# Kernel optimization log

Measured on AMD Instinct MI355X. Metric: run time of the kernel, lower is better.

Reference implementation:

```python
import jax, jax.numpy as jnp
import numpy as np

B, L, E, H = 4, 512, 2048, 32
S = E // H  # head_size = 64
EXTRA_MAA, EXTRA_DECAY = 32, 64
EPS = 1e-5


def setup_inputs() -> dict:
    key = jax.random.key(0)
    ks = jax.random.split(key, 24)
    rn = lambda k, shp, s=1.0: jax.random.normal(k, shp, dtype=jnp.float32) * s
    return dict(
        x=rn(ks[0], (B, L, E)),
        state=rn(ks[1], (B, 2 + S, E), 0.1),
        ln1_w=jnp.ones((E,), jnp.float32), ln1_b=jnp.zeros((E,), jnp.float32),
        ln2_w=jnp.ones((E,), jnp.float32), ln2_b=jnp.zeros((E,), jnp.float32),
        maa_x=rn(ks[2], (E,), 0.02),
        maa_w1=rn(ks[3], (E, 5 * EXTRA_MAA), 0.02),
        maa_w2=rn(ks[4], (5, EXTRA_MAA, E), 0.02),
        maa_stack=rn(ks[5], (5, E), 0.02),          # [k,w,v,r,g] time_maa vectors
        time_decay=rn(ks[6], (E,), 0.5),
        decay_w1=rn(ks[7], (E, EXTRA_DECAY), 0.02),
        decay_w2=rn(ks[8], (EXTRA_DECAY, E), 0.02),
        faaaa=rn(ks[9], (H, S), 0.1),
        Wr=rn(ks[10], (E, E), 0.02), Wk=rn(ks[11], (E, E), 0.02),
        Wv=rn(ks[12], (E, E), 0.02), Wg=rn(ks[13], (E, E), 0.02),
        Wo=rn(ks[14], (E, E), 0.02),
        gn_w=jnp.ones((E,), jnp.float32), gn_b=jnp.zeros((E,), jnp.float32),
        ffn_maa_k=rn(ks[15], (E,), 0.02), ffn_maa_r=rn(ks[16], (E,), 0.02),
        ffn_Wk=rn(ks[17], (E, E), 0.02), ffn_Wr=rn(ks[18], (E, E), 0.02),
        ffn_Wv=rn(ks[19], (E, E), 0.02),
        i=0,
    )


def _ln(x, w, b):
    m = jnp.mean(x, axis=-1, keepdims=True)
    v = jnp.mean((x - m) ** 2, axis=-1, keepdims=True)
    return (x - m) * jax.lax.rsqrt(v + EPS) * w + b


def _token_shift(xn, prev_row):
    # sx_lerp[t] = x[t-1] - x[t], with state row as x[-1]
    first = (prev_row - xn[:, 0])[:, None]
    rest = xn[:, :-1] - xn[:, 1:]
    return jnp.concatenate([first, rest], axis=1)


def reference(x, state, ln1_w, ln1_b, ln2_w, ln2_b, maa_x, maa_w1, maa_w2,
              maa_stack, time_decay, decay_w1, decay_w2, faaaa,
              Wr, Wk, Wv, Wg, Wo, gn_w, gn_b,
              ffn_maa_k, ffn_maa_r, ffn_Wk, ffn_Wr, ffn_Wv, i):
    b, l = x.shape[0], x.shape[1]
    i0 = (2 + S) * i + 0
    i1 = (2 + S) * i + 1

    # ---- time mixing (parallel) ----
    xn = _ln(x, ln1_w, ln1_b)
    sx = _token_shift(xn, state[:, i1])
    xxx = jnp.tanh((xn + sx * maa_x) @ maa_w1).reshape(b, l, 5, 1, EXTRA_MAA)
    xxx = jnp.matmul(xxx, maa_w2).reshape(b, l, 5, E)   # [B,L,5,E]
    x5 = xn[:, :, None] + sx[:, :, None] * (maa_stack + xxx)

    w = jnp.exp(-jnp.exp(time_decay + jnp.tanh(x5[:, :, 1] @ decay_w1) @ decay_w2))
    w = w.reshape(b, l, H, S)
    r = (x5[:, :, 3] @ Wr.T).reshape(b, l, H, S)
    k = (x5[:, :, 0] @ Wk.T).reshape(b, l, H, S)
    v = (x5[:, :, 2] @ Wv.T).reshape(b, l, H, S)
    g = jax.nn.silu(x5[:, :, 4] @ Wg.T)                 # [B,L,E]

    s0 = state[:, (2 + S) * i + 2:(2 + S) * (i + 1)].reshape(b, H, S, S)
    u = faaaa[None, :, :, None]                         # [1,H,S,1]

    def step(s, rkvw):
        r_t, k_t, v_t, w_t = rkvw                      # each [B,H,S]
        a = k_t[:, :, :, None] * v_t[:, :, None, :]    # [B,H,S,S] outer product
        out = jnp.einsum('bhk,bhkd->bhd', r_t, u * a + s)
        return a + w_t[:, :, :, None] * s, out

    xs = tuple(jnp.moveaxis(t, 1, 0) for t in (r, k, v, w))
    _, outs = jax.lax.scan(step, s0, xs)               # outs [L,B,H,S]
    att = jnp.moveaxis(outs, 0, 1).reshape(b, l, E)

    # group norm over each head's channels
    a4 = att.reshape(b, l, H, S)
    m = jnp.mean(a4, axis=-1, keepdims=True)
    var = jnp.mean((a4 - m) ** 2, axis=-1, keepdims=True)
    att = ((a4 - m) * jax.lax.rsqrt(var + EPS)).reshape(b, l, E) * gn_w + gn_b
    x = x + (att * g) @ Wo.T

    # ---- channel mixing (parallel) ----
    xn2 = _ln(x, ln2_w, ln2_b)
    sx2 = _token_shift(xn2, state[:, i0])
    xk = xn2 + sx2 * ffn_maa_k
    xr = xn2 + sx2 * ffn_maa_r
    rr = jax.nn.sigmoid(xr @ ffn_Wr.T)
    kk = jnp.square(jax.nn.relu(xk @ ffn_Wk.T))
    x = x + rr * (kk @ ffn_Wv.T)
    return x
```

## Files before the change

kernel.cpp:

```cpp
#include <hip/hip_runtime.h>

#define EE 2048
#define LL 512
#define BBATCH 4
#define HH 32
#define SS 64
#define EPSF 1e-5f
static constexpr size_t NEL = (size_t)BBATCH * LL * EE;

typedef __attribute__((ext_vector_type(8))) short short8;
typedef __attribute__((ext_vector_type(4))) float f32x4;

__device__ __forceinline__ unsigned short f2bf(float f) {
  union { float f; unsigned u; } x; x.f = f;
  return (unsigned short)((x.u + 0x7fffu + ((x.u >> 16) & 1u)) >> 16);
}

__device__ __forceinline__ void gload_lds16(const unsigned short* g, unsigned short* l) {
  __builtin_amdgcn_global_load_lds((const __attribute__((address_space(1))) void*)g,
                                   (__attribute__((address_space(3))) void*)l, 16, 0, 0);
}

template <int N>
__device__ __forceinline__ void wait_vmcnt_n() {
  if constexpr (N == 4) asm volatile("s_waitcnt vmcnt(4)" ::: "memory");
  else if constexpr (N == 6) asm volatile("s_waitcnt vmcnt(6)" ::: "memory");
  else if constexpr (N == 8) asm volatile("s_waitcnt vmcnt(8)" ::: "memory");
  else asm volatile("s_waitcnt vmcnt(0)" ::: "memory");
}

struct CvArgs {
  const float* s[4];
  unsigned short* d[4];
};
__global__ void __launch_bounds__(256) f2bf_batch(CvArgs a, int n4) {
  int z = blockIdx.y;
  int idx = blockIdx.x * 256 + threadIdx.x;
  if (idx >= n4) return;
  float4 v = ((const float4*)a.s[z])[idx];
  ushort4 o;
  o.x = f2bf(v.x); o.y = f2bf(v.y); o.z = f2bf(v.z); o.w = f2bf(v.w);
  ((ushort4*)a.d[z])[idx] = o;
}

__global__ void __launch_bounds__(256) wprep_kernel(const float* __restrict__ w1,
                                                    const float* __restrict__ w2,
                                                    const float* __restrict__ d1,
                                                    const float* __restrict__ d2,
                                                    unsigned short* __restrict__ w1T,
                                                    unsigned short* __restrict__ w2cat,
                                                    unsigned short* __restrict__ dw1T,
                                                    unsigned short* __restrict__ dw2T) {
  const int N0 = 256 * 2048;
  const int N1 = 10240 * 160;
  const int N2 = 128 * 2048;
  const int N3 = 2048 * 128;
  int id = blockIdx.x * 256 + threadIdx.x;
  if (id < N0) {
    int n = id >> 11, k = id & 2047;
    float v = (n < 160) ? w1[(size_t)k * 160 + n] : 0.f;
    w1T[id] = f2bf(v);
    return;
  }
  id -= N0;
  if (id < N1) {
    int n = id / 160, kq = id - n * 160;
    int j = n >> 11, e = n & 2047;
    float v = ((kq >> 5) == j) ? w2[(size_t)kq * 2048 + e] : 0.f;
    w2cat[id] = f2bf(v);
    return;
  }
  id -= N1;
  if (id < N2) {
    int n = id >> 11, k = id & 2047;
    float v = (n < 64) ? d1[(size_t)k * 64 + n] : 0.f;
    dw1T[id] = f2bf(v);
    return;
  }
  id -= N2;
  if (id < N3) {
    int n = id >> 7, k = id & 127;
    float v = (k < 64) ? d2[(size_t)k * 2048 + n] : 0.f;
    dw2T[id] = f2bf(v);
  }
}

template <int SIDE>
__global__ void __launch_bounds__(256) ln_shift_kernel(
    const float* __restrict__ x, const float* __restrict__ state, const int* __restrict__ ip,
    const float* __restrict__ lnw, const float* __restrict__ lnb,
    const float* __restrict__ mA, const float* __restrict__ mB,
    float* __restrict__ xn_out, unsigned short* __restrict__ o1,
    float* __restrict__ sx_out, unsigned short* __restrict__ o2) {
  __shared__ float red[8];
  int tok = blockIdx.x;
  int b = tok >> 9, t = tok & 511;
  int tid = threadIdx.x;
  int e = tid * 8;
  size_t base = (size_t)tok * EE;
  float c[8], p[8];
  *(float4*)&c[0] = *(const float4*)&x[base + e];
  *(float4*)&c[4] = *(const float4*)&x[base + e + 4];
  bool hasp = (t != 0);
  if (hasp) {
    *(float4*)&p[0] = *(const float4*)&x[base - EE + e];
    *(float4*)&p[4] = *(const float4*)&x[base - EE + e + 4];
  } else {
    const float* srow = state + ((size_t)b * (2 + SS) + (size_t)(2 + SS) * (*ip) +
                                 (SIDE == 0 ? 1 : 0)) * EE;
    *(float4*)&p[0] = *(const float4*)&srow[e];
    *(float4*)&p[4] = *(const float4*)&srow[e + 4];
  }
  float sc = 0.f, sp = 0.f;
#pragma unroll
  for (int j = 0; j < 8; ++j) { sc += c[j]; sp += p[j]; }
#pragma unroll
  for (int off = 32; off >= 1; off >>= 1) {
    sc += __shfl_xor(sc, off);
    sp += __shfl_xor(sp, off);
  }
  if ((tid & 63) == 0) { red[tid >> 6] = sc; red[4 + (tid >> 6)] = sp; }
  __syncthreads();
  float mc = (red[0] + red[1] + red[2] + red[3]) * (1.f / EE);
  float mp = (red[4] + red[5] + red[6] + red[7]) * (1.f / EE);
  __syncthreads();
  float qc = 0.f, qp = 0.f;
#pragma unroll
  for (int j = 0; j < 8; ++j) {
    float dc = c[j] - mc, dp = p[j] - mp;
    qc += dc * dc; qp += dp * dp;
  }
#pragma unroll
  for (int off = 32; off >= 1; off >>= 1) {
    qc += __shfl_xor(qc, off);
    qp += __shfl_xor(qp, off);
  }
  if ((tid & 63) == 0) { red[tid >> 6] = qc; red[4 + (tid >> 6)] = qp; }
  __syncthreads();
  float rc = rsqrtf((red[0] + red[1] + red[2] + red[3]) * (1.f / EE) + EPSF);
  float rp = rsqrtf((red[4] + red[5] + red[6] + red[7]) * (1.f / EE) + EPSF);
  float wv[8], bv[8], av[8], bv2[8];
  *(float4*)&wv[0] = *(const float4*)&lnw[e];
  *(float4*)&wv[4] = *(const float4*)&lnw[e + 4];
  *(float4*)&bv[0] = *(const float4*)&lnb[e];
  *(float4*)&bv[4] = *(const float4*)&lnb[e + 4];
  *(float4*)&av[0] = *(const float4*)&mA[e];
  *(float4*)&av[4] = *(const float4*)&mA[e + 4];
  if (SIDE == 1) {
    *(float4*)&bv2[0] = *(const float4*)&mB[e];
    *(float4*)&bv2[4] = *(const float4*)&mB[e + 4];
  }
  float cn[8], sxv[8];
#pragma unroll
  for (int j = 0; j < 8; ++j) {
    float cnj = (c[j] - mc) * rc * wv[j] + bv[j];
    float pnj = hasp ? ((p[j] - mp) * rp * wv[j] + bv[j]) : p[j];
    cn[j] = cnj;
    sxv[j] = pnj - cnj;
  }
  if constexpr (SIDE == 0) {
    *(float4*)&xn_out[base + e] = *(float4*)&cn[0];
    *(float4*)&xn_out[base + e + 4] = *(float4*)&cn[4];
    *(float4*)&sx_out[base + e] = *(float4*)&sxv[0];
    *(float4*)&sx_out[base + e + 4] = *(float4*)&sxv[4];
    ushort4 xo0, xo1;
    xo0.x = f2bf(cn[0] + sxv[0] * av[0]); xo0.y = f2bf(cn[1] + sxv[1] * av[1]);
    xo0.z = f2bf(cn[2] + sxv[2] * av[2]); xo0.w = f2bf(cn[3] + sxv[3] * av[3]);
    xo1.x = f2bf(cn[4] + sxv[4] * av[4]); xo1.y = f2bf(cn[5] + sxv[5] * av[5]);
    xo1.z = f2bf(cn[6] + sxv[6] * av[6]); xo1.w = f2bf(cn[7] + sxv[7] * av[7]);
    *(ushort4*)&o1[base + e] = xo0;
    *(ushort4*)&o1[base + e + 4] = xo1;
  } else {
    ushort4 k0, k1, r0, r1;
    k0.x = f2bf(cn[0] + sxv[0] * av[0]); k0.y = f2bf(cn[1] + sxv[1] * av[1]);
    k0.z = f2bf(cn[2] + sxv[2] * av[2]); k0.w = f2bf(cn[3] + sxv[3] * av[3]);
    k1.x = f2bf(cn[4] + sxv[4] * av[4]); k1.y = f2bf(cn[5] + sxv[5] * av[5]);
    k1.z = f2bf(cn[6] + sxv[6] * av[6]); k1.w = f2bf(cn[7] + sxv[7] * av[7]);
    r0.x = f2bf(cn[0] + sxv[0] * bv2[0]); r0.y = f2bf(cn[1] + sxv[1] * bv2[1]);
    r0.z = f2bf(cn[2] + sxv[2] * bv2[2]); r0.w = f2bf(cn[3] + sxv[3] * bv2[3]);
    r1.x = f2bf(cn[4] + sxv[4] * bv2[4]); r1.y = f2bf(cn[5] + sxv[5] * bv2[5]);
    r1.z = f2bf(cn[6] + sxv[6] * bv2[6]); r1.w = f2bf(cn[7] + sxv[7] * bv2[7]);
    *(ushort4*)&o1[base + e] = k0;
    *(ushort4*)&o1[base + e + 4] = k1;
    *(ushort4*)&o2[base + e] = r0;
    *(ushort4*)&o2[base + e + 4] = r1;
  }
}

template <int ROWS, int BK, int NT>
__device__ __forceinline__ void stage_mat(const unsigned short* __restrict__ base, int ld,
                                          int k0, unsigned short* dst) {
  constexpr int GPR = BK / 8;
  constexpr int L = ROWS * GPR / NT;
  int tid = threadIdx.x;
#pragma unroll
  for (int r = 0; r < L; ++r) {
    int g = r * NT + tid;
    int row = g / GPR, p = g & (GPR - 1);
    int lg = p ^ (row & (GPR - 1));
    gload_lds16(base + (size_t)row * ld + k0 + lg * 8, &dst[g * 8]);
  }
}

template <int BM, int BN, int BK, int NT, int WM, int WN>
__device__ __forceinline__ void gemm_core(const unsigned short* __restrict__ A, int lda,
                                          const unsigned short* __restrict__ W, int ldw,
                                          int K, int bm, int bn, unsigned short* AsAll,
                                          unsigned short* BsAll,
                                          f32x4 (&acc)[BM / WM / 16][BN / WN / 16],
                                          int& m0o, int& n0o) {
  constexpr int FM = BM / WM / 16, FN = BN / WN / 16, KS = BK / 32;
  constexpr int GPR = BK / 8;
  constexpr int NLD = (BM + BN) * GPR / NT;
  int tid = threadIdx.x;
  int wave = tid >> 6, lane = tid & 63;
  int wm = wave / WN, wn = wave % WN;
  const unsigned short* Abase = A + (size_t)bm * BM * lda;
  const unsigned short* Bbase = W + (size_t)bn * BN * ldw;
  const int T = K / BK;
  stage_mat<BM, BK, NT>(Abase, lda, 0, AsAll);
  stage_mat<BN, BK, NT>(Bbase, ldw, 0, BsAll);
  {
    int k1 = (T > 1) ? BK : 0;
    stage_mat<BM, BK, NT>(Abase, lda, k1, AsAll + BM * BK);
    stage_mat<BN, BK, NT>(Bbase, ldw, k1, BsAll + BN * BK);
  }
  int q = lane >> 4;
  int rA = wm * (BM / WM) + (lane & 15);
  int rB = wn * (BN / WN) + (lane & 15);
  int xrA = rA & (GPR - 1), xrB = rB & (GPR - 1);
  for (int t = 0; t < T; ++t) {
    unsigned short* As = AsAll + (t & 1) * (BM * BK);
    unsigned short* Bs = BsAll + (t & 1) * (BN * BK);
    wait_vmcnt_n<NLD>();
    __builtin_amdgcn_s_barrier();
    __builtin_amdgcn_sched_barrier(0);
    short8 av[KS][FM], bv[KS][FN];
#pragma unroll
    for (int ks = 0; ks < KS; ++ks) {
#pragma unroll
      for (int f = 0; f < FM; f++) {
        int p = (ks * 4 + q) ^ xrA;
        av[ks][f] = *(const short8*)&As[(rA + f * 16) * BK + p * 8];
      }
#pragma unroll
      for (int f = 0; f < FN; f++) {
        int p = (ks * 4 + q) ^ xrB;
        bv[ks][f] = *(const short8*)&Bs[(rB + f * 16) * BK + p * 8];
      }
    }
    asm volatile("s_waitcnt lgkmcnt(0)" ::: "memory");
    __builtin_amdgcn_sched_barrier(0);
    __builtin_amdgcn_s_barrier();
    int tn = t + 2;
    if (tn >= T) tn -= T;
    stage_mat<BM, BK, NT>(Abase, lda, tn * BK, As);
    stage_mat<BN, BK, NT>(Bbase, ldw, tn * BK, Bs);
    __builtin_amdgcn_s_setprio(1);
#pragma unroll
    for (int ks = 0; ks < KS; ++ks)
#pragma unroll
      for (int fm = 0; fm < FM; fm++)
#pragma unroll
        for (int fn = 0; fn < FN; fn++)
          acc[fm][fn] = __builtin_amdgcn_mfma_f32_16x16x32_bf16(av[ks][fm], bv[ks][fn],
                                                                acc[fm][fn], 0, 0, 0);
    __builtin_amdgcn_s_setprio(0);
  }
  m0o = bm * BM + wm * (BM / WM);
  n0o = bn * BN + wn * (BN / WN);
}

template <int FM, int FN, typename F>
__device__ __forceinline__ void epi_loop(f32x4 (&acc)[FM][FN], int m0, int n0, F f) {
  int lane = threadIdx.x & 63;
  int rl = (lane >> 4) * 4, cl = lane & 15;
#pragma unroll
  for (int fm = 0; fm < FM; fm++)
#pragma unroll
    for (int fn = 0; fn < FN; fn++)
#pragma unroll
      for (int q = 0; q < 4; q++)
        f(m0 + fm * 16 + rl + q, n0 + fn * 16 + cl, acc[fm][fn][q]);
}

template <int MODE, int BM, int BN, int BK>
__global__ void __launch_bounds__(256) gemm_bt(const unsigned short* __restrict__ A, int lda,
                                               const unsigned short* __restrict__ W, int ldw,
                                               int K, int NB, void* __restrict__ Cout, int ldc,
                                               const float* __restrict__ p1,
                                               const float* __restrict__ p2,
                                               const float* __restrict__ p3) {
  __shared__ __align__(16) unsigned short As[2 * BM * BK];
  __shared__ __align__(16) unsigned short Bs[2 * BN * BK];
  int nwg = gridDim.x, bid = blockIdx.x;
  int qd = nwg >> 3;
  int wg = (bid & 7) * qd + (bid >> 3);
  int bm = wg / NB, bn = wg - bm * NB;
  f32x4 acc[BM / 32][BN / 32] = {};
  int m0, n0;
  gemm_core<BM, BN, BK, 256, 2, 2>(A, lda, W, ldw, K, bm, bn, As, Bs, acc, m0, n0);
  epi_loop(acc, m0, n0, [&](int m, int n, float val) {
    size_t o = (size_t)m * ldc + n;
    if constexpr (MODE == 2) {
      ((float*)Cout)[o] = p1[o] + val;
    } else if constexpr (MODE == 3) {
      ((float*)Cout)[o] = p1[o] + val * (1.f / (1.f + expf(-p2[o])));
    } else if constexpr (MODE == 5) {
      ((unsigned short*)Cout)[o] = f2bf(tanhf(val));
    } else if constexpr (MODE == 6) {
      ((float*)Cout)[o] = expf(-expf(p1[n] + val));
    } else {
      int j = n >> 11, e = n & 2047;
      size_t oe = (size_t)m * EE + e;
      float xv = p1[oe];
      float sv = p2[oe];
      float st = p3[(size_t)j * EE + e];
      ((unsigned short*)Cout)[(size_t)j * NEL + oe] = f2bf(xv + sv * (st + val));
    }
  });
}

struct Proj4Args {
  const unsigned short* A[4];
  const unsigned short* W[4];
  float* C[4];
};
__global__ void __launch_bounds__(512, 1) gemm_proj4(Proj4Args args) {
  __shared__ __align__(16) unsigned short As[2 * 256 * 64];
  __shared__ __align__(16) unsigned short Bs[2 * 256 * 64];
  int bid = blockIdx.x;
  int xcd = bid & 7;
  int z = xcd >> 1;
  int tile = ((xcd & 1) << 5) + (bid >> 3);
  int bm = tile >> 3, bn = tile & 7;
  f32x4 acc[8][4] = {};
  int m0, n0;
  gemm_core<256, 256, 64, 512, 2, 4>(args.A[z], EE, args.W[z], EE, EE, bm, bn, As, Bs, acc,
                                     m0, n0);
  float* C = args.C[z];
  bool silu = (z == 3);
  epi_loop(acc, m0, n0, [&](int m, int n, float val) {
    size_t o = (size_t)m * EE + n;
    C[o] = silu ? (val / (1.f + expf(-val))) : val;
  });
}

__global__ void __launch_bounds__(256) gemm_ffn2(const unsigned short* A0,
                                                 const unsigned short* A1,
                                                 const unsigned short* W0,
                                                 const unsigned short* W1, float* C0,
                                                 unsigned short* C1) {
  __shared__ __align__(16) unsigned short As[2 * 128 * 64];
  __shared__ __align__(16) unsigned short Bs[2 * 128 * 64];
  int bid = blockIdx.x;
  int xcd = bid & 7;
  int z = xcd >> 2;
  int tile = ((xcd & 3) << 6) + (bid >> 3);
  int bm = tile >> 4, bn = tile & 15;
  f32x4 acc[4][4] = {};
  int m0, n0;
  gemm_core<128, 128, 64, 256, 2, 2>(z ? A1 : A0, EE, z ? W1 : W0, EE, EE, bm, bn, As, Bs,
                                     acc, m0, n0);
  epi_loop(acc, m0, n0, [&](int m, int n, float val) {
    size_t o = (size_t)m * EE + n;
    if (z == 0) {
      C0[o] = val;
    } else {
      float rv = fmaxf(val, 0.f);
      C1[o] = f2bf(rv * rv);
    }
  });
}

__global__ void __launch_bounds__(512) scan_kernel(const float* __restrict__ r,
                                                   const float* __restrict__ k,
                                                   const float* __restrict__ v,
                                                   const float* __restrict__ w,
                                                   const float* __restrict__ state,
                                                   const float* __restrict__ faaaa,
                                                   const int* __restrict__ ip,
                                                   float* __restrict__ att) {
  __shared__ float bR[2][8][32], bK[2][8][32], bW[2][8][32];
  __shared__ float bV[2][8][64];
  __shared__ float part[8][8][64];
  int blk = blockIdx.x;
  int bh = blk >> 1, kh = blk & 1;
  int b = bh >> 5, h = bh & 31;
  int tid = threadIdx.x, wv = tid >> 6, lane = tid & 63;
  int klocal = wv * 4;
  int k0w = kh * 32 + klocal;
  int ii = *ip;
  const float* sb = state + ((size_t)b * (2 + SS) + (size_t)(2 + SS) * ii + 2) * EE;
  float s_[4], u_[4];
#pragma unroll
  for (int q = 0; q < 4; ++q) {
    int kk_ = k0w + q;
    s_[q] = sb[(size_t)(2 * h + (kk_ >> 5)) * EE + (kk_ & 31) * 64 + lane];
    u_[q] = faaaa[h * 64 + kk_];
  }
  size_t base = (size_t)b * LL * EE + (size_t)h * 64;
  int c = tid;
  bool ld = c < 320;
  int lt = c / 40, r40 = c - lt * 40;
  int la = (r40 < 24) ? (r40 >> 3) : 3;
  int lcG = (r40 < 24) ? (kh * 32 + (r40 & 7) * 4) : ((r40 - 24) * 4);
  int lcL = (r40 < 24) ? ((r40 & 7) * 4) : ((r40 - 24) * 4);
  const float* lsrc = nullptr;
  if (ld) {
    const float* arr = (la == 0) ? r : (la == 1) ? k : (la == 2) ? w : v;
    lsrc = arr + base + (size_t)lt * EE + lcG;
    float4 v0 = *(const float4*)lsrc;
    if (la == 0) *(float4*)&bR[0][lt][lcL] = v0;
    else if (la == 1) *(float4*)&bK[0][lt][lcL] = v0;
    else if (la == 2) *(float4*)&bW[0][lt][lcL] = v0;
    else *(float4*)&bV[0][lt][lcL] = v0;
  }
  __syncthreads();
  for (int g = 0; g < 64; ++g) {
    int cb = g & 1;
    float4 nv;
    if (ld && g < 63) nv = *(const float4*)(lsrc + (size_t)(g + 1) * 8 * EE);
#pragma unroll
    for (int t = 0; t < 8; ++t) {
      float vv = bV[cb][t][lane];
      float acc = 0.f;
#pragma unroll
      for (int q = 0; q < 4; ++q) {
        float rk = bR[cb][t][klocal + q];
        float kk2 = bK[cb][t][klocal + q];
        float wk = bW[cb][t][klocal + q];
        float a = kk2 * vv;
        acc = fmaf(rk, fmaf(u_[q], a, s_[q]), acc);
        s_[q] = fmaf(wk, s_[q], a);
      }
      part[t][wv][lane] = acc;
    }
    if (ld && g < 63) {
      int nb = cb ^ 1;
      if (la == 0) *(float4*)&bR[nb][lt][lcL] = nv;
      else if (la == 1) *(float4*)&bK[nb][lt][lcL] = nv;
      else if (la == 2) *(float4*)&bW[nb][lt][lcL] = nv;
      else *(float4*)&bV[nb][lt][lcL] = nv;
    }
    __syncthreads();
    {
      int t = tid >> 6, d = tid & 63;
      float tot = part[t][0][d] + part[t][1][d] + part[t][2][d] + part[t][3][d] +
                  part[t][4][d] + part[t][5][d] + part[t][6][d] + part[t][7][d];
      atomicAdd(&att[base + (size_t)(g * 8 + t) * EE + d], tot);
    }
    __syncthreads();
  }
}

__global__ void __launch_bounds__(256) gn_gate_kernel(const float* __restrict__ att,
                                                      const float* __restrict__ g,
                                                      const float* __restrict__ gnw,
                                                      const float* __restrict__ gnb,
                                                      unsigned short* __restrict__ attg) {
  int tok = blockIdx.x, tid = threadIdx.x;
  int h = tid >> 3, j = tid & 7;
  size_t base = (size_t)tok * EE + h * 64 + j * 8;
  int e = h * 64 + j * 8;
  float4 a0 = *(const float4*)&att[base];
  float4 a1 = *(const float4*)&att[base + 4];
  float s = a0.x + a0.y + a0.z + a0.w + a1.x + a1.y + a1.z + a1.w;
  s += __shfl_xor(s, 1); s += __shfl_xor(s, 2); s += __shfl_xor(s, 4);
  float mean = s * (1.f / 64.f);
  float d, q = 0.f;
  d = a0.x - mean; q += d * d; d = a0.y - mean; q += d * d;
  d = a0.z - mean; q += d * d; d = a0.w - mean; q += d * d;
  d = a1.x - mean; q += d * d; d = a1.y - mean; q += d * d;
  d = a1.z - mean; q += d * d; d = a1.w - mean; q += d * d;
  q += __shfl_xor(q, 1); q += __shfl_xor(q, 2); q += __shfl_xor(q, 4);
  float rstd = rsqrtf(q * (1.f / 64.f) + EPSF);
  float4 w0 = *(const float4*)&gnw[e], w1 = *(const float4*)&gnw[e + 4];
  float4 b0 = *(const float4*)&gnb[e], b1 = *(const float4*)&gnb[e + 4];
  float4 g0 = *(const float4*)&g[base], g1 = *(const float4*)&g[base + 4];
  ushort4 o0, o1;
  o0.x = f2bf(((a0.x - mean) * rstd * w0.x + b0.x) * g0.x);
  o0.y = f2bf(((a0.y - mean) * rstd * w0.y + b0.y) * g0.y);
  o0.z = f2bf(((a0.z - mean) * rstd * w0.z + b0.z) * g0.z);
  o0.w = f2bf(((a0.w - mean) * rstd * w0.w + b0.w) * g0.w);
  o1.x = f2bf(((a1.x - mean) * rstd * w1.x + b1.x) * g1.x);
  o1.y = f2bf(((a1.y - mean) * rstd * w1.y + b1.y) * g1.y);
  o1.z = f2bf(((a1.z - mean) * rstd * w1.z + b1.z) * g1.z);
  o1.w = f2bf(((a1.w - mean) * rstd * w1.w + b1.w) * g1.w);
  *(ushort4*)&attg[base] = o0;
  *(ushort4*)&attg[base + 4] = o1;
}

extern "C" void kernel_launch(void* const* d_in, const int* in_sizes, int n_in,
                              void* d_out, int out_size, void* d_ws, size_t ws_size,
                              hipStream_t stream) {
  const float* x = (const float*)d_in[0];
  const float* state = (const float*)d_in[1];
  const float* ln1_w = (const float*)d_in[2];
  const float* ln1_b = (const float*)d_in[3];
  const float* ln2_w = (const float*)d_in[4];
  const float* ln2_b = (const float*)d_in[5];
  const float* maa_x = (const float*)d_in[6];
  const float* maa_w1 = (const float*)d_in[7];
  const float* maa_w2 = (const float*)d_in[8];
  const float* maa_stack = (const float*)d_in[9];
  const float* time_decay = (const float*)d_in[10];
  const float* decay_w1 = (const float*)d_in[11];
  const float* decay_w2 = (const float*)d_in[12];
  const float* faaaa = (const float*)d_in[13];
  const float* Wr = (const float*)d_in[14];
  const float* Wk = (const float*)d_in[15];
  const float* Wv = (const float*)d_in[16];
  const float* Wg = (const float*)d_in[17];
  const float* Wo = (const float*)d_in[18];
  const float* gn_w = (const float*)d_in[19];
  const float* gn_b = (const float*)d_in[20];
  const float* ffn_maa_k = (const float*)d_in[21];
  const float* ffn_maa_r = (const float*)d_in[22];
  const float* fWk = (const float*)d_in[23];
  const float* fWr = (const float*)d_in[24];
  const float* fWv = (const float*)d_in[25];
  const int* ip = (const int*)d_in[26];

  char* ws = (char*)d_ws;
  const size_t MB1 = 1024 * 1024;
  unsigned short* WB0 = (unsigned short*)ws;
  unsigned short* WB1 = (unsigned short*)(ws + 8 * MB1);
  float* xn = (float*)(ws + 16 * MB1);
  unsigned short* x5b = (unsigned short*)(ws + 32 * MB1);
  float* wbuf = (float*)(ws + 72 * MB1);
  float* rbuf = (float*)(ws + 88 * MB1);
  float* kbuf = (float*)(ws + 104 * MB1);
  float* vbuf = (float*)(ws + 120 * MB1);
  float* gbuf = (float*)(ws + 136 * MB1);
  char* smalls = ws + 152 * MB1;
  unsigned short* th = (unsigned short*)smalls;
  unsigned short* w1T = (unsigned short*)(smalls + 1 * MB1);
  unsigned short* w2cat = (unsigned short*)(smalls + 2 * MB1);
  unsigned short* dw1T = (unsigned short*)(smalls + 5376 * 1024);
  unsigned short* dw2T = (unsigned short*)(smalls + 5888 * 1024);
  unsigned short* dt = (unsigned short*)(smalls + 6400 * 1024);

  unsigned short* xxm = (unsigned short*)wbuf;
  float* sx = gbuf;
  float* att = xn;
  unsigned short* WB2 = (unsigned short*)xn;
  unsigned short* WB3 = WB2 + NEL;
  unsigned short* attg = x5b;
  unsigned short* xkb = x5b;
  unsigned short* fWvB = x5b + 1 * NEL;
  unsigned short* xrb = x5b + 2 * NEL;
  unsigned short* kkb = x5b + 3 * NEL;
  unsigned short* fWkB = x5b + 4 * NEL;
  float* rrraw = wbuf;

  const int thr = 256;
  const int nconv = (int)(NEL / 4);

  ln_shift_kernel<0><<<BBATCH * LL, thr, 0, stream>>>(x, state, ip, ln1_w, ln1_b, maa_x,
                                                      nullptr, xn, xxm, sx, nullptr);
  wprep_kernel<<<10496, thr, 0, stream>>>(maa_w1, maa_w2, decay_w1, decay_w2, w1T, w2cat,
                                          dw1T, dw2T);
  gemm_bt<5, 64, 64, 64><<<128, thr, 0, stream>>>(xxm, 2048, w1T, 2048, 2048, 4, th, 256,
                                                  nullptr, nullptr, nullptr);
  gemm_bt<7, 128, 128, 32><<<1280, thr, 0, stream>>>(th, 256, w2cat, 160, 160, 80, x5b, 0,
                                                     xn, sx, maa_stack);
  gemm_bt<5, 64, 64, 64><<<64, thr, 0, stream>>>(x5b + 1 * NEL, 2048, dw1T, 2048, 2048, 2,
                                                 dt, 128, nullptr, nullptr, nullptr);
  gemm_bt<6, 128, 128, 64><<<256, thr, 0, stream>>>(dt, 128, dw2T, 128, 128, 16, wbuf, 2048,
                                                    time_decay, nullptr, nullptr);
  {
    CvArgs ca;
    ca.s[0] = Wk; ca.d[0] = WB0;
    ca.s[1] = Wv; ca.d[1] = WB1;
    ca.s[2] = Wr; ca.d[2] = WB2;
    ca.s[3] = Wg; ca.d[3] = WB3;
    f2bf_batch<<<dim3(4096, 4), thr, 0, stream>>>(ca, nconv);
  }
  {
    Proj4Args pa;
    pa.A[0] = x5b + 0 * NEL; pa.W[0] = WB0; pa.C[0] = kbuf;
    pa.A[1] = x5b + 2 * NEL; pa.W[1] = WB1; pa.C[1] = vbuf;
    pa.A[2] = x5b + 3 * NEL; pa.W[2] = WB2; pa.C[2] = rbuf;
    pa.A[3] = x5b + 4 * NEL; pa.W[3] = WB3; pa.C[3] = gbuf;
    gemm_proj4<<<256, 512, 0, stream>>>(pa);
  }
  {
    CvArgs cb;
    cb.s[0] = Wo; cb.d[0] = WB0;
    cb.s[1] = fWr; cb.d[1] = WB1;
    cb.s[2] = fWk; cb.d[2] = fWkB;
    cb.s[3] = fWv; cb.d[3] = fWvB;
    f2bf_batch<<<dim3(4096, 4), thr, 0, stream>>>(cb, nconv);
  }
  (void)hipMemsetAsync(att, 0, NEL * sizeof(float), stream);
  scan_kernel<<<256, 512, 0, stream>>>(rbuf, kbuf, vbuf, wbuf, state, faaaa, ip, att);
  gn_gate_kernel<<<BBATCH * LL, thr, 0, stream>>>(att, gbuf, gn_w, gn_b, attg);
  gemm_bt<2, 128, 64, 64><<<512, thr, 0, stream>>>(attg, 2048, WB0, 2048, 2048, 32,
                                                   (float*)d_out, 2048, x, nullptr, nullptr);
  ln_shift_kernel<1><<<BBATCH * LL, thr, 0, stream>>>((const float*)d_out, state, ip, ln2_w,
                                                      ln2_b, ffn_maa_k, ffn_maa_r, nullptr,
                                                      xkb, nullptr, xrb);
  gemm_ffn2<<<512, thr, 0, stream>>>(xrb, xkb, WB1, fWkB, rrraw, kkb);
  gemm_bt<3, 128, 64, 64><<<512, thr, 0, stream>>>(kkb, 2048, fWvB, 2048, 2048, 32,
                                                   (float*)d_out, 2048, (const float*)d_out,
                                                   rrraw, nullptr);
}
```

Baseline: 434.7 us.

## Split scan work by value dimension, dropping atomics and the memset

The WKV scan kernel now gives each block half of the value dimension (d) rather than half of the key dimension. That lets each output element be written by exactly one block with a plain store, so the atomicAdd and the memset of the att buffer go away. The scan now stages 16 timesteps per group in one interleaved LDS buffer and reduces the two key halves within a wave using a shuffle. Barriers wait only on LDS counters rather than doing a full syncthreads. In exchange, each block has to load all of r, k and w for its head, which adds global traffic. The padded partial-sum array is meant to reduce LDS bank conflicts.

```diff
diff --git a/kernel.cpp b/kernel.cpp
--- a/kernel.cpp
+++ b/kernel.cpp
@@ -27,6 +27,12 @@
   else if constexpr (N == 6) asm volatile("s_waitcnt vmcnt(6)" ::: "memory");
   else if constexpr (N == 8) asm volatile("s_waitcnt vmcnt(8)" ::: "memory");
   else asm volatile("s_waitcnt vmcnt(0)" ::: "memory");
+}
+
+__device__ __forceinline__ void barrier_lgkm_only() {
+  asm volatile("s_waitcnt lgkmcnt(0)" ::: "memory");
+  __builtin_amdgcn_sched_barrier(0);
+  __builtin_amdgcn_s_barrier();
 }
 
 struct CvArgs {
@@ -373,6 +379,7 @@
   });
 }
 
+#define GS 16
 __global__ void __launch_bounds__(512) scan_kernel(const float* __restrict__ r,
                                                    const float* __restrict__ k,
                                                    const float* __restrict__ v,
@@ -381,76 +388,85 @@
                                                    const float* __restrict__ faaaa,
                                                    const int* __restrict__ ip,
                                                    float* __restrict__ att) {
-  __shared__ float bR[2][8][32], bK[2][8][32], bW[2][8][32];
-  __shared__ float bV[2][8][64];
-  __shared__ float part[8][8][64];
+  __shared__ float bufAll[2][GS * 224];
+  __shared__ float part[GS][8][34];
   int blk = blockIdx.x;
-  int bh = blk >> 1, kh = blk & 1;
+  int bh = blk >> 1, dh = blk & 1;
   int b = bh >> 5, h = bh & 31;
   int tid = threadIdx.x, wv = tid >> 6, lane = tid & 63;
-  int klocal = wv * 4;
-  int k0w = kh * 32 + klocal;
+  int d32 = lane & 31;
+  int k0w = wv * 8 + (lane >> 5) * 4;
+  int dfull = dh * 32 + d32;
   int ii = *ip;
   const float* sb = state + ((size_t)b * (2 + SS) + (size_t)(2 + SS) * ii + 2) * EE;
   float s_[4], u_[4];
 #pragma unroll
   for (int q = 0; q < 4; ++q) {
     int kk_ = k0w + q;
-    s_[q] = sb[(size_t)(2 * h + (kk_ >> 5)) * EE + (kk_ & 31) * 64 + lane];
+    s_[q] = sb[(size_t)(2 * h + (kk_ >> 5)) * EE + (kk_ & 31) * 64 + dfull];
     u_[q] = faaaa[h * 64 + kk_];
   }
   size_t base = (size_t)b * LL * EE + (size_t)h * 64;
-  int c = tid;
-  bool ld = c < 320;
-  int lt = c / 40, r40 = c - lt * 40;
-  int la = (r40 < 24) ? (r40 >> 3) : 3;
-  int lcG = (r40 < 24) ? (kh * 32 + (r40 & 7) * 4) : ((r40 - 24) * 4);
-  int lcL = (r40 < 24) ? ((r40 & 7) * 4) : ((r40 - 24) * 4);
-  const float* lsrc = nullptr;
-  if (ld) {
-    const float* arr = (la == 0) ? r : (la == 1) ? k : (la == 2) ? w : v;
-    lsrc = arr + base + (size_t)lt * EE + lcG;
-    float4 v0 = *(const float4*)lsrc;
-    if (la == 0) *(float4*)&bR[0][lt][lcL] = v0;
-    else if (la == 1) *(float4*)&bK[0][lt][lcL] = v0;
-    else if (la == 2) *(float4*)&bW[0][lt][lcL] = v0;
-    else *(float4*)&bV[0][lt][lcL] = v0;
-  }
-  __syncthreads();
-  for (int g = 0; g < 64; ++g) {
+  int i0 = tid;
+  int row0 = i0 / 56, j0 = i0 - row0 * 56;
+  const float* a0; int off0, gc0;
+  if (j0 < 16) { a0 = r; off0 = j0 * 4; gc0 = j0 * 4; }
+  else if (j0 < 32) { a0 = k; off0 = 64 + (j0 - 16) * 4; gc0 = (j0 - 16) * 4; }
+  else if (j0 < 48) { a0 = w; off0 = 128 + (j0 - 32) * 4; gc0 = (j0 - 32) * 4; }
+  else { a0 = v; off0 = 192 + (j0 - 48) * 4; gc0 = dh * 32 + (j0 - 48) * 4; }
+  const float* lsrc0 = a0 + base + (size_t)row0 * EE + gc0;
+  int loff0 = row0 * 224 + off0;
+  bool has1 = (tid < 384);
+  int i1 = tid + 512;
+  int row1 = i1 / 56, j1 = i1 - row1 * 56;
+  const float* a1; int off1, gc1;
+  if (j1 < 16) { a1 = r; off1 = j1 * 4; gc1 = j1 * 4; }
+  else if (j1 < 32) { a1 = k; off1 = 64 + (j1 - 16) * 4; gc1 = (j1 - 16) * 4; }
+  else if (j1 < 48) { a1 = w; off1 = 128 + (j1 - 32) * 4; gc1 = (j1 - 32) * 4; }
+  else { a1 = v; off1 = 192 + (j1 - 48) * 4; gc1 = dh * 32 + (j1 - 48) * 4; }
+  const float* lsrc1 = a1 + base + (size_t)row1 * EE + gc1;
+  int loff1 = row1 * 224 + off1;
+  *(float4*)&bufAll[0][loff0] = *(const float4*)lsrc0;
+  if (has1) *(float4*)&bufAll[0][loff1] = *(const float4*)lsrc1;
+  barrier_lgkm_only();
+  for (int g = 0; g < 32; ++g) {
     int cb = g & 1;
-    float4 nv;
-    if (ld && g < 63) nv = *(const float4*)(lsrc + (size_t)(g + 1) * 8 * EE);
-#pragma unroll
-    for (int t = 0; t < 8; ++t) {
-      float vv = bV[cb][t][lane];
+    float4 nv0, nv1;
+    if (g < 31) {
+      nv0 = *(const float4*)(lsrc0 + (size_t)(g + 1) * GS * EE);
+      if (has1) nv1 = *(const float4*)(lsrc1 + (size_t)(g + 1) * GS * EE);
+    }
+    const float* buf = bufAll[cb];
+#pragma unroll
+    for (int t = 0; t < GS; ++t) {
+      const float* rowp = buf + t * 224;
+      float vv = rowp[192 + d32];
       float acc = 0.f;
 #pragma unroll
       for (int q = 0; q < 4; ++q) {
-        float rk = bR[cb][t][klocal + q];
-        float kk2 = bK[cb][t][klocal + q];
-        float wk = bW[cb][t][klocal + q];
+        float rk = rowp[k0w + q];
+        float kk2 = rowp[64 + k0w + q];
+        float wk = rowp[128 + k0w + q];
         float a = kk2 * vv;
         acc = fmaf(rk, fmaf(u_[q], a, s_[q]), acc);
         s_[q] = fmaf(wk, s_[q], a);
       }
-      part[t][wv][lane] = acc;
+      acc += __shfl_xor(acc, 32);
+      if (lane < 32) part[t][wv][d32] = acc;
     }
-    if (ld && g < 63) {
-      int nb = cb ^ 1;
-      if (la == 0) *(float4*)&bR[nb][lt][lcL] = nv;
-      else if (la == 1) *(float4*)&bK[nb][lt][lcL] = nv;
-      else if (la == 2) *(float4*)&bW[nb][lt][lcL] = nv;
-      else *(float4*)&bV[nb][lt][lcL] = nv;
+    if (g < 31) {
+      float* nb = bufAll[cb ^ 1];
+      *(float4*)&nb[loff0] = nv0;
+      if (has1) *(float4*)&nb[loff1] = nv1;
     }
-    __syncthreads();
+    barrier_lgkm_only();
     {
-      int t = tid >> 6, d = tid & 63;
-      float tot = part[t][0][d] + part[t][1][d] + part[t][2][d] + part[t][3][d] +
-                  part[t][4][d] + part[t][5][d] + part[t][6][d] + part[t][7][d];
-      atomicAdd(&att[base + (size_t)(g * 8 + t) * EE + d], tot);
+      int tt = tid >> 5, dd = tid & 31;
+      float tot = part[tt][0][dd] + part[tt][1][dd] + part[tt][2][dd] + part[tt][3][dd] +
+                  part[tt][4][dd] + part[tt][5][dd] + part[tt][6][dd] + part[tt][7][dd];
+      att[base + (size_t)(g * GS + tt) * EE + dh * 32 + dd] = tot;
     }
-    __syncthreads();
+    barrier_lgkm_only();
   }
 }
 
@@ -593,7 +609,6 @@
     cb.s[3] = fWv; cb.d[3] = fWvB;
     f2bf_batch<<<dim3(4096, 4), thr, 0, stream>>>(cb, nconv);
   }
-  (void)hipMemsetAsync(att, 0, NEL * sizeof(float), stream);
   scan_kernel<<<256, 512, 0, stream>>>(rbuf, kbuf, vbuf, wbuf, state, faaaa, ip, att);
   gn_gate_kernel<<<BBATCH * LL, thr, 0, stream>>>(att, gbuf, gn_w, gn_b, attg);
   gemm_bt<2, 128, 64, 64><<<512, thr, 0, stream>>>(attg, 2048, WB0, 2048, 2048, 32,
```

Measured after the change: 415.6 us. 1.05x faster.
